# Performance work log

Measured on AMD Instinct MI355X. Metric: run time of the kernel, lower is better.

## Reference

```python
import jax, jax.numpy as jnp
import numpy as np

H, DH, M, ITERS, DIM = 8, 64, 256, 6, 512
SCALE = DH ** -0.5


def setup_inputs() -> dict:
    key = jax.random.key(0)
    ks = jax.random.split(key, 6)
    b, n, nz = 4, 8192, 4096  # multiples of M=256 -> padding branch is a no-op
    s = DIM ** -0.5
    x = jax.random.normal(ks[0], (b, n, DIM), jnp.float32)
    z = jax.random.normal(ks[1], (b, nz, DIM), jnp.float32)
    W_q = jax.random.normal(ks[2], (DIM, H * DH), jnp.float32) * s      # to_qkv[0] (no bias)
    W_kv = jax.random.normal(ks[3], (DIM, 2 * H * DH), jnp.float32) * s  # to_qkv[1] (no bias)
    W_out = jax.random.normal(ks[4], (H * DH, DIM), jnp.float32) * s     # to_out Linear
    b_out = jax.random.normal(ks[5], (DIM,), jnp.float32) * 0.01
    return {"x": x, "z": z, "W_q": W_q, "W_kv": W_kv, "W_out": W_out, "b_out": b_out}


def moore_penrose_pinv(a, iters=ITERS):
    # Newton-Schulz iterative pseudo-inverse (faithful to moore_penrose_iter_pinv)
    abs_a = jnp.abs(a)
    col = abs_a.sum(axis=-1)
    row = abs_a.sum(axis=-2)
    zt = jnp.swapaxes(a, -1, -2) / (jnp.max(col) * jnp.max(row))
    I = jnp.eye(a.shape[-1], dtype=a.dtype)
    for _ in range(iters):
        az = a @ zt
        zt = 0.25 * zt @ (13.0 * I - az @ (15.0 * I - az @ (7.0 * I - az)))
    return zt


def reference(x, z, W_q, W_kv, W_out, b_out):
    b, n, _ = x.shape
    nz = z.shape[1]
    l, lz = n // M, nz // M  # landmark group sizes (n, nz are multiples of M)

    # projections (dropout=0.1 is inactive at inference; self.norm is never applied in forward)
    q = (x @ W_q).reshape(b, n, H, DH).transpose(0, 2, 1, 3) * SCALE   # [b,h,n,dh]
    kv = z @ W_kv
    k = kv[..., : H * DH].reshape(b, nz, H, DH).transpose(0, 2, 1, 3)  # [b,h,nz,dh]
    v = kv[..., H * DH :].reshape(b, nz, H, DH).transpose(0, 2, 1, 3)  # [b,h,nz,dh]

    # landmarks: mean over groups of l (resp. lz) consecutive tokens
    q_land = q.reshape(b, H, M, l, DH).sum(axis=3) / l    # [b,h,M,dh]
    k_land = k.reshape(b, H, M, lz, DH).sum(axis=3) / lz  # [b,h,M,dh]

    sim1 = jnp.einsum('bhid,bhjd->bhij', q, k_land)       # [b,h,n,M]
    sim2 = jnp.einsum('bhid,bhjd->bhij', q_land, k_land)  # [b,h,M,M]
    sim3 = jnp.einsum('bhid,bhjd->bhij', q_land, k)       # [b,h,M,nz]
    attn1 = jax.nn.softmax(sim1, axis=-1)
    attn2 = jax.nn.softmax(sim2, axis=-1)
    attn3 = jax.nn.softmax(sim3, axis=-1)

    attn2_inv = moore_penrose_pinv(attn2)
    # (attn1 @ attn2_inv) @ (attn3 @ v) computed small-first for efficiency; same math
    out = attn1 @ (attn2_inv @ (attn3 @ v))               # [b,h,n,dh]  (residual=False)

    out = out.transpose(0, 2, 1, 3).reshape(b, n, H * DH)
    out = out @ W_out + b_out
    return x + out
```

## Files before the change

### kernel.cpp

```cpp
#include <hip/hip_runtime.h>

typedef unsigned short u16;
typedef __attribute__((ext_vector_type(8))) short bf16x8s;
typedef __attribute__((ext_vector_type(4))) float f32x4;

#define DEV static __device__ __forceinline__

DEV float b2f(u16 v) { return __uint_as_float(((unsigned)v) << 16); }
DEV u16 f2b(float f) {
  unsigned r;
  asm("v_cvt_pk_bf16_f32 %0, %1, %1" : "=v"(r) : "v"(f));
  return (u16)r;
}
DEV unsigned f2b2(float a, float b) {
  unsigned r;
  asm("v_cvt_pk_bf16_f32 %0, %1, %2" : "=v"(r) : "v"(a), "v"(b));
  return r;
}

#define GLL(gp, lp)                                                            \
  __builtin_amdgcn_global_load_lds(                                            \
      (const __attribute__((address_space(1))) unsigned int*)(gp),             \
      (__attribute__((address_space(3))) unsigned int*)(lp), 16, 0, 0)

#define MFMA __builtin_amdgcn_mfma_f32_16x16x32_bf16

__global__ __launch_bounds__(256) void k_f2bxz(const float* __restrict__ x,
                                               const float* __restrict__ z,
                                               u16* __restrict__ xb,
                                               u16* __restrict__ zb) {
  long i = (long)blockIdx.x * 256 + threadIdx.x;
  const float* src;
  u16* dst;
  long j;
  if (i < 4194304) { src = x; dst = xb; j = i; }
  else { src = z; dst = zb; j = i - 4194304; }
  float4 v = *(const float4*)(src + j * 4);
  unsigned* d = (unsigned*)(dst + j * 4);
  d[0] = f2b2(v.x, v.y);
  d[1] = f2b2(v.z, v.w);
}

__global__ __launch_bounds__(256) void k_wt3(const float* __restrict__ Wq,
                                             const float* __restrict__ Wkv,
                                             const float* __restrict__ Wo,
                                             u16* __restrict__ wqt,
                                             u16* __restrict__ wkvt,
                                             u16* __restrict__ wot) {
  int e = blockIdx.x * 256 + threadIdx.x;
  const float* W;
  u16* Wt;
  int N, le;
  if (e < 262144) { W = Wq; Wt = wqt; N = 512; le = e; }
  else if (e < 786432) { W = Wkv; Wt = wkvt; N = 1024; le = e - 262144; }
  else { W = Wo; Wt = wot; N = 512; le = e - 786432; }
  int nn = le >> 9, kk = le & 511;
  Wt[le] = f2b(W[(long)kk * N + nn]);
}

template <int MODE>
__global__ __launch_bounds__(256, 2) void k_gemm128(
    const u16* __restrict__ A, const u16* __restrict__ Bm, void* __restrict__ C0,
    void* __restrict__ C1, const float* __restrict__ xres,
    const float* __restrict__ bias, int K) {
  const int nwg = gridDim.x * gridDim.y;
  const int orig = blockIdx.y * gridDim.x + blockIdx.x;
  const int qq = nwg >> 3, rr = nwg & 7;
  const int xcd = orig & 7, loc = orig >> 3;
  const int swz = (xcd < rr ? xcd * (qq + 1) : rr * (qq + 1) + (xcd - rr) * qq) + loc;
  const int m0 = (swz / gridDim.x) << 7, n0 = (swz % gridDim.x) << 7;
  const int t = threadIdx.x, lane = t & 63, w = t >> 6;
  const int wm = (w >> 1) << 6, wn = (w & 1) << 6;
  const int fr = lane & 15, g = lane >> 4;
  __shared__ u16 sh[16384];
  u16* As = sh;
  u16* Bs = sh + 8192;
  f32x4 acc[4][4] = {};
  const int srow = t >> 3, scs = t & 7;
  for (int k0 = 0; k0 < K; k0 += 64) {
    __syncthreads();
#pragma unroll
    for (int i = 0; i < 4; ++i) {
      int row = srow + (i << 5), cs = scs;
      GLL(A + (long)(m0 + row) * K + k0 + ((cs ^ (row & 7)) << 3),
          &As[(i << 11) + (w << 9)]);
      GLL(Bm + (long)(n0 + row) * K + k0 + ((cs ^ (row & 7)) << 3),
          &Bs[(i << 11) + (w << 9)]);
    }
    __syncthreads();
#pragma unroll
    for (int ks = 0; ks < 2; ++ks) {
      bf16x8s af[4], bf[4];
#pragma unroll
      for (int fi = 0; fi < 4; ++fi) {
        int row = wm + fi * 16 + fr;
        af[fi] = *(const bf16x8s*)((const char*)As + row * 128 +
                                   (((ks * 4 + g) ^ (row & 7)) << 4));
      }
#pragma unroll
      for (int fj = 0; fj < 4; ++fj) {
        int row = wn + fj * 16 + fr;
        bf[fj] = *(const bf16x8s*)((const char*)Bs + row * 128 +
                                   (((ks * 4 + g) ^ (row & 7)) << 4));
      }
#pragma unroll
      for (int fi = 0; fi < 4; ++fi)
#pragma unroll
        for (int fj = 0; fj < 4; ++fj)
          acc[fi][fj] = MFMA(af[fi], bf[fj], acc[fi][fj], 0, 0, 0);
    }
  }
  const int crow = g << 2;
  if (MODE == 2) {
#pragma unroll
    for (int fi = 0; fi < 4; ++fi)
#pragma unroll
      for (int fj = 0; fj < 4; ++fj)
#pragma unroll
        for (int r = 0; r < 4; ++r) {
          int row = m0 + wm + fi * 16 + crow + r;
          int col = n0 + wn + fj * 16 + fr;
          long idx = ((long)row << 9) + col;
          ((float*)C0)[idx] = acc[fi][fj][r] + xres[idx] + bias[col];
        }
  } else {
    __syncthreads();
    char* Cs = (char*)sh;
    const float scale = (MODE == 0) ? 0.125f : 1.f;
#pragma unroll
    for (int fi = 0; fi < 4; ++fi)
#pragma unroll
      for (int fj = 0; fj < 4; ++fj)
#pragma unroll
        for (int r = 0; r < 4; ++r) {
          int row = wm + fi * 16 + crow + r;
          int colb = (wn + fj * 16 + fr) << 1;
          *(u16*)(Cs + ((row * 256 + colb) ^ ((row & 7) << 4))) =
              f2b(acc[fi][fj][r] * scale);
        }
    __syncthreads();
    const bool vt = (MODE == 1) && (n0 >= 512);
    if (!vt) {
#pragma unroll
      for (int i = 0; i < 8; ++i) {
        int seg = (i << 8) + t;
        int row = seg >> 4, cs = seg & 15;
        bf16x8s v = *(const bf16x8s*)(Cs +
                        ((row * 256 + (cs << 4)) ^ ((row & 7) << 4)));
        int m = m0 + row;
        int colg = n0 + (cs << 3);
        int h = colg >> 6, dh0 = colg & 63;
        if (MODE == 0) {
          int b = m >> 13, n = m & 8191;
          *(bf16x8s*)((u16*)C0 + ((((long)(b * 8 + h)) << 13) + n) * 64 + dh0) = v;
        } else {
          int b = m >> 12, nz = m & 4095;
          *(bf16x8s*)((u16*)C0 + ((((long)(b * 8 + h)) << 12) + nz) * 64 + dh0) = v;
        }
      }
    } else {
#pragma unroll
      for (int i = 0; i < 8; ++i) {
        int seg = (i << 8) + t;
        int col = seg & 127;
        int r0 = (seg >> 7) << 3;
        bf16x8s v;
#pragma unroll
        for (int j = 0; j < 8; ++j) {
          int rr = r0 + j;
          v[j] = *(const short*)(Cs + ((rr * 256 + (col << 1)) ^ ((rr & 7) << 4)));
        }
        int m = m0 + r0;
        int b = m >> 12, nz0 = m & 4095;
        int c2 = n0 + col - 512;
        int h = c2 >> 6, dh = c2 & 63;
        *(bf16x8s*)((u16*)C1 + ((((long)(b * 8 + h) * 64 + dh)) << 12) + nz0) = v;
      }
    }
  }
}

__global__ __launch_bounds__(256) void k_land2(const u16* __restrict__ qb,
                                               const u16* __restrict__ kb,
                                               u16* __restrict__ qlh,
                                               u16* __restrict__ qll,
                                               u16* __restrict__ klh,
                                               u16* __restrict__ kll) {
  int pidx = blockIdx.x * 4 + (threadIdx.x >> 6);
  const u16* src;
  u16 *hi, *lo;
  int ntok, l;
  float inv;
  if (pidx < 8192) { src = qb; hi = qlh; lo = qll; ntok = 8192; l = 32; inv = 1.f / 32.f; }
  else { src = kb; hi = klh; lo = kll; ntok = 4096; l = 16; inv = 1.f / 16.f; pidx -= 8192; }
  int d = threadIdx.x & 63;
  int bh = pidx >> 8, m = pidx & 255;
  const u16* s = src + ((long)bh * ntok + (long)m * l) * 64 + d;
  float sum = 0.f;
  for (int j = 0; j < l; ++j) sum += b2f(s[j * 64]);
  sum *= inv;
  long o = ((long)bh * 256 + m) * 64 + d;
  u16 h = f2b(sum);
  hi[o] = h;
  lo[o] = f2b(sum - b2f(h));
}

__global__ __launch_bounds__(256, 2) void k_sim2(
    const u16* __restrict__ qlh, const u16* __restrict__ qll,
    const u16* __restrict__ klh, const u16* __restrict__ kll,
    float* __restrict__ attn2, u16* __restrict__ aNhi, u16* __restrict__ aNlo) {
  const int rb = blockIdx.x, bh = blockIdx.y;
  const int t = threadIdx.x, lane = t & 63, w = t >> 6;
  const int fr = lane & 15, g = lane >> 4;
  __shared__ char lds[65536];
  {
    const u16* kh = klh + (long)bh * 16384;
    const u16* kl = kll + (long)bh * 16384;
    int srow8 = lane >> 3, cs7 = lane & 7;
#pragma unroll
    for (int i = 0; i < 8; ++i) {
      int slab = w * 8 + i;
      int krow = slab * 8 + srow8;
      GLL(kh + krow * 64 + ((cs7 ^ (krow & 7)) << 3), lds + slab * 1024);
      GLL(kl + krow * 64 + ((cs7 ^ (krow & 7)) << 3), lds + 32768 + slab * 1024);
    }
  }
  long qoff = ((long)bh * 256 + rb * 64 + w * 16 + fr) * 64;
  bf16x8s qh0 = *(const bf16x8s*)(qlh + qoff + g * 8);
  bf16x8s qh1 = *(const bf16x8s*)(qlh + qoff + 32 + g * 8);
  bf16x8s ql0 = *(const bf16x8s*)(qll + qoff + g * 8);
  bf16x8s ql1 = *(const bf16x8s*)(qll + qoff + 32 + g * 8);
  __syncthreads();
  f32x4 s[16];
#pragma unroll
  for (int c = 0; c < 16; ++c) {
    int j = (c << 4) + fr;
    int o0 = j * 128 + ((g ^ (j & 7)) << 4);
    int o1 = j * 128 + (((4 + g) ^ (j & 7)) << 4);
    bf16x8s kh0 = *(const bf16x8s*)(lds + o0);
    bf16x8s kh1 = *(const bf16x8s*)(lds + o1);
    bf16x8s kl0 = *(const bf16x8s*)(lds + 32768 + o0);
    bf16x8s kl1 = *(const bf16x8s*)(lds + 32768 + o1);
    f32x4 zz = {};
    zz = MFMA(qh0, kh0, zz, 0, 0, 0);
    zz = MFMA(qh1, kh1, zz, 0, 0, 0);
    zz = MFMA(qh0, kl0, zz, 0, 0, 0);
    zz = MFMA(qh1, kl1, zz, 0, 0, 0);
    zz = MFMA(ql0, kh0, zz, 0, 0, 0);
    zz = MFMA(ql1, kh1, zz, 0, 0, 0);
    s[c] = zz;
  }
  float li[4];
#pragma unroll
  for (int r = 0; r < 4; ++r) {
    float m = s[0][r];
#pragma unroll
    for (int c = 1; c < 16; ++c) m = fmaxf(m, s[c][r]);
    m = fmaxf(m, __shfl_xor(m, 1, 64));
    m = fmaxf(m, __shfl_xor(m, 2, 64));
    m = fmaxf(m, __shfl_xor(m, 4, 64));
    m = fmaxf(m, __shfl_xor(m, 8, 64));
    float l = 0.f;
#pragma unroll
    for (int c = 0; c < 16; ++c) {
      float e = __expf(s[c][r] - m);
      s[c][r] = e;
      l += e;
    }
    l += __shfl_xor(l, 1, 64);
    l += __shfl_xor(l, 2, 64);
    l += __shfl_xor(l, 4, 64);
    l += __shfl_xor(l, 8, 64);
    li[r] = 1.f / l;
  }
#pragma unroll
  for (int c = 0; c < 16; ++c)
#pragma unroll
    for (int r = 0; r < 4; ++r) {
      int row = rb * 64 + w * 16 + (g << 2) + r;
      int col = (c << 4) + fr;
      long idx = ((long)bh << 16) + ((long)row << 8) + col;
      float p = s[c][r] * li[r];
      attn2[idx] = p;
      u16 h = f2b(p);
      aNhi[idx] = h;
      aNlo[idx] = f2b(p - b2f(h));
    }
}

__global__ __launch_bounds__(256) void k_colmax(const float* __restrict__ attn2,
                                                unsigned* __restrict__ cmax) {
  int bh = blockIdx.x, j = threadIdx.x, lane = j & 63, w = j >> 6;
  const float* p = attn2 + ((long)bh << 16) + j;
  float s = 0.f;
  for (int m = 0; m < 256; ++m) s += p[m * 256];
  float mx = s;
  for (int o = 1; o < 64; o <<= 1) mx = fmaxf(mx, __shfl_xor(mx, o, 64));
  __shared__ float r1[4];
  if (lane == 0) r1[w] = mx;
  __syncthreads();
  if (j == 0) {
    mx = fmaxf(fmaxf(r1[0], r1[1]), fmaxf(r1[2], r1[3]));
    atomicMax(cmax, __float_as_uint(mx));
  }
}

__global__ __launch_bounds__(256, 2) void k_t1part(
    const u16* __restrict__ qlb, const u16* __restrict__ kb,
    const u16* __restrict__ vtb, float* __restrict__ opart,
    float* __restrict__ pm_, float* __restrict__ pl_) {
  int orig = blockIdx.x;
  int xcd = orig & 7, idx = orig >> 3;
  int p = xcd * 16 + (idx >> 2);
  int rb = idx & 3;
  int bh = p >> 2, kc = p & 3;
  const int t = threadIdx.x, lane = t & 63, w = t >> 6;
  const int fr = lane & 15, g = lane >> 4;
  __shared__ char lds[65536];
  const u16* qrow = qlb + ((long)bh * 256 + rb * 64 + w * 16 + fr) * 64;
  bf16x8s qa0 = *(const bf16x8s*)(qrow + g * 8);
  bf16x8s qa1 = *(const bf16x8s*)(qrow + 32 + g * 8);
  f32x4 o[4] = {};
  float m[4] = {-3e38f, -3e38f, -3e38f, -3e38f};
  float l[4] = {};
  const long kbase = (long)bh * 262144;
  for (int cc = 0; cc < 4; ++cc) {
    int c0 = kc * 1024 + cc * 256;
    __syncthreads();
#pragma unroll
    for (int i = 0; i < 8; ++i) {
      int seg = (i << 8) + t, row = seg >> 3, cs = seg & 7;
      GLL(kb + kbase + (long)(c0 + row) * 64 + ((cs ^ (row & 7)) << 3),
          lds + (i << 12) + (w << 10));
    }
#pragma unroll
    for (int i = 0; i < 8; ++i) {
      int seg = (i << 8) + t, row = seg >> 5, cs = seg & 31;
      GLL(vtb + kbase + (long)row * 4096 + c0 + ((cs ^ (row & 7)) << 3),
          lds + 32768 + (i << 12) + (w << 10));
    }
    __syncthreads();
    f32x4 s[16];
#pragma unroll
    for (int c = 0; c < 16; ++c) {
      int j = c * 16 + fr;
      bf16x8s b0 = *(const bf16x8s*)(lds + j * 128 + ((g ^ (j & 7)) << 4));
      bf16x8s b1 = *(const bf16x8s*)(lds + j * 128 + (((4 + g) ^ (j & 7)) << 4));
      f32x4 zz = {};
      zz = MFMA(qa0, b0, zz, 0, 0, 0);
      zz = MFMA(qa1, b1, zz, 0, 0, 0);
      s[c] = zz;
    }
    float sc[4];
#pragma unroll
    for (int r = 0; r < 4; ++r) {
      float pm = s[0][r];
#pragma unroll
      for (int c = 1; c < 16; ++c) pm = fmaxf(pm, s[c][r]);
      pm = fmaxf(pm, __shfl_xor(pm, 1, 64));
      pm = fmaxf(pm, __shfl_xor(pm, 2, 64));
      pm = fmaxf(pm, __shfl_xor(pm, 4, 64));
      pm = fmaxf(pm, __shfl_xor(pm, 8, 64));
      float mn = fmaxf(m[r], pm);
      sc[r] = __expf(m[r] - mn);
      m[r] = mn;
    }
#pragma unroll
    for (int r = 0; r < 4; ++r) {
      float su = 0.f;
#pragma unroll
      for (int c = 0; c < 16; ++c) {
        float e = __expf(s[c][r] - m[r]);
        s[c][r] = e;
        su += e;
      }
      su += __shfl_xor(su, 1, 64);
      su += __shfl_xor(su, 2, 64);
      su += __shfl_xor(su, 4, 64);
      su += __shfl_xor(su, 8, 64);
      l[r] = l[r] * sc[r] + su;
    }
#pragma unroll
    for (int d = 0; d < 4; ++d)
#pragma unroll
      for (int r = 0; r < 4; ++r) o[d][r] *= sc[r];
    __syncthreads();
#pragma unroll
    for (int c = 0; c < 16; ++c)
#pragma unroll
      for (int r = 0; r < 4; ++r) {
        int row = (w << 4) + (g << 2) + r;
        int byin = (c << 5) + (fr << 1);
        *(u16*)(lds + row * 512 + (byin ^ ((row & 7) << 4))) = f2b(s[c][r]);
      }
    asm volatile("s_waitcnt lgkmcnt(0)" ::: "memory");
    __builtin_amdgcn_sched_barrier(0);
#pragma unroll
    for (int ss = 0; ss < 8; ++ss) {
      int prow = (w << 4) + fr;
      bf16x8s ap = *(const bf16x8s*)(lds + prow * 512 +
                                     (((ss * 64) + (g << 4)) ^ ((prow & 7) << 4)));
#pragma unroll
      for (int d = 0; d < 4; ++d) {
        int dh = (d << 4) + fr;
        bf16x8s bv = *(const bf16x8s*)(lds + 32768 + dh * 512 +
                                       (((ss * 4 + g) ^ (dh & 7)) << 4));
        o[d] = MFMA(ap, bv, o[d], 0, 0, 0);
      }
    }
  }
  __syncthreads();
  float* lf = (float*)lds;
#pragma unroll
  for (int d = 0; d < 4; ++d)
#pragma unroll
    for (int r = 0; r < 4; ++r)
      lf[((w << 4) + (g << 2) + r) * 76 + (d << 4) + fr] = o[d][r];
  __syncthreads();
  const long pb = (long)(bh * 4 + kc) * 256 + rb * 64;
#pragma unroll
  for (int i = 0; i < 4; ++i) {
    int row = i * 16 + (t >> 4);
    int c4 = (t & 15) << 2;
    float4 v = *(const float4*)&lf[row * 76 + c4];
    *(float4*)&opart[(pb + row) * 64 + c4] = v;
  }
  if (fr == 0) {
#pragma unroll
    for (int r = 0; r < 4; ++r) {
      int lr = (w << 4) + (g << 2) + r;
      pm_[pb + lr] = m[r];
      pl_[pb + lr] = l[r];
    }
  }
}

__global__ __launch_bounds__(256) void k_t1merge(
    const float* __restrict__ opart, const float* __restrict__ pm_,
    const float* __restrict__ pl_, u16* __restrict__ T1thi,
    u16* __restrict__ T1tlo) {
  const int rb = blockIdx.x, bh = blockIdx.y;
  const int t = threadIdx.x;
#pragma unroll
  for (int rp = 0; rp < 4; ++rp) {
    int row = rb * 64 + rp * 16 + (t >> 4);
    int dh4 = (t & 15) << 2;
    float pmv[4], M = -3e38f;
#pragma unroll
    for (int i = 0; i < 4; ++i) {
      pmv[i] = pm_[(long)(bh * 4 + i) * 256 + row];
      M = fmaxf(M, pmv[i]);
    }
    float L = 0.f, wt[4];
#pragma unroll
    for (int i = 0; i < 4; ++i) {
      wt[i] = __expf(pmv[i] - M);
      L += pl_[(long)(bh * 4 + i) * 256 + row] * wt[i];
    }
    float4 acc = {0.f, 0.f, 0.f, 0.f};
#pragma unroll
    for (int i = 0; i < 4; ++i) {
      float4 v = *(const float4*)&opart[((long)(bh * 4 + i) * 256 + row) * 64 + dh4];
      acc.x += v.x * wt[i]; acc.y += v.y * wt[i];
      acc.z += v.z * wt[i]; acc.w += v.w * wt[i];
    }
    float invL = 1.f / L;
    float vv[4] = {acc.x * invL, acc.y * invL, acc.z * invL, acc.w * invL};
#pragma unroll
    for (int e = 0; e < 4; ++e) {
      int dh = dh4 + e;
      long idx = (long)bh * 16384 + (long)dh * 256 + row;
      u16 h = f2b(vv[e]);
      T1thi[idx] = h;
      T1tlo[idx] = f2b(vv[e] - b2f(h));
    }
  }
}

template <int NP>
__global__ __launch_bounds__(256) void k_nn_mfma(
    const u16* __restrict__ Ahi, const u16* __restrict__ Alo,
    const u16* __restrict__ Bthi, const u16* __restrict__ Btlo,
    u16* __restrict__ CNhi, u16* __restrict__ CNlo,
    u16* __restrict__ CThi, u16* __restrict__ CTlo,
    int Nc, float sab, float sa, float cdiag) {
  const int bz = blockIdx.z;
  const long offA = (long)bz << 16;
  const long offB = (long)bz * ((long)Nc << 8);
  const int m0 = blockIdx.y << 6, n0 = blockIdx.x << 6;
  const int t = threadIdx.x, lane = t & 63, w = t >> 6;
  const int wm = (w >> 1) << 5, wn = (w & 1) << 5;
  const int fr = lane & 15, g = lane >> 4;
  __shared__ u16 lds[16384];
  u16* LAh = lds;
  u16* LAl = lds + 4096;
  u16* LBh = lds + 8192;
  u16* LBl = lds + 12288;
  f32x4 acc[2][2] = {};
  const int srow8 = lane >> 3, cs = lane & 7;
  for (int k0 = 0; k0 < 256; k0 += 64) {
    __syncthreads();
#pragma unroll
    for (int j = 0; j < 2; ++j) {
      int slab = w * 2 + j;
      int row = slab * 8 + srow8;
      long asrc = offA + (long)(m0 + row) * 256 + k0 + ((cs ^ (row & 7)) << 3);
      long bsrc = offB + (long)(n0 + row) * 256 + k0 + ((cs ^ (row & 7)) << 3);
      GLL(Ahi + asrc, LAh + slab * 512);
      GLL(Bthi + bsrc, LBh + slab * 512);
      if (NP == 3) {
        GLL(Alo + asrc, LAl + slab * 512);
        GLL(Btlo + bsrc, LBl + slab * 512);
      }
    }
    __syncthreads();
#pragma unroll
    for (int ks = 0; ks < 2; ++ks) {
      const int ra0 = wm + fr, ra1 = wm + 16 + fr;
      const int rb0 = wn + fr, rb1 = wn + 16 + fr;
#define RD(base, row) \
  (*(const bf16x8s*)((const char*)(base) + (row) * 128 + (((ks * 4 + g) ^ ((row) & 7)) << 4)))
      bf16x8s ah0 = RD(LAh, ra0), ah1 = RD(LAh, ra1);
      bf16x8s bh0 = RD(LBh, rb0), bh1 = RD(LBh, rb1);
      acc[0][0] = MFMA(ah0, bh0, acc[0][0], 0, 0, 0);
      acc[0][1] = MFMA(ah0, bh1, acc[0][1], 0, 0, 0);
      acc[1][0] = MFMA(ah1, bh0, acc[1][0], 0, 0, 0);
      acc[1][1] = MFMA(ah1, bh1, acc[1][1], 0, 0, 0);
      if (NP == 3) {
        bf16x8s al0 = RD(LAl, ra0), al1 = RD(LAl, ra1);
        bf16x8s bl0 = RD(LBl, rb0), bl1 = RD(LBl, rb1);
        acc[0][0] = MFMA(ah0, bl0, acc[0][0], 0, 0, 0);
        acc[0][0] = MFMA(al0, bh0, acc[0][0], 0, 0, 0);
        acc[0][1] = MFMA(ah0, bl1, acc[0][1], 0, 0, 0);
        acc[0][1] = MFMA(al0, bh1, acc[0][1], 0, 0, 0);
        acc[1][0] = MFMA(ah1, bl0, acc[1][0], 0, 0, 0);
        acc[1][0] = MFMA(al1, bh0, acc[1][0], 0, 0, 0);
        acc[1][1] = MFMA(ah1, bl1, acc[1][1], 0, 0, 0);
        acc[1][1] = MFMA(al1, bh1, acc[1][1], 0, 0, 0);
      }
#undef RD
    }
  }
  const int crow = g << 2;
  const long offC = (long)bz * ((long)Nc << 8);
#pragma unroll
  for (int i = 0; i < 2; ++i)
#pragma unroll
    for (int j = 0; j < 2; ++j)
#pragma unroll
      for (int r = 0; r < 4; ++r) {
        int row = m0 + wm + i * 16 + crow + r;
        int col = n0 + wn + j * 16 + fr;
        float v = sab * acc[i][j][r];
        if (sa != 0.f) {
          long ai = offA + ((long)row << 8) + col;
          v += sa * (b2f(Ahi[ai]) + b2f(Alo[ai]));
        }
        if (row == col) v += cdiag;
        if (CNhi) {
          long ci = offC + (long)row * Nc + col;
          u16 h = f2b(v);
          if (CNlo) { CNhi[ci] = h; CNlo[ci] = f2b(v - b2f(h)); }
          else CNhi[ci] = h;
        }
        if (CThi) {
          long ti = offC + ((long)col << 8) + row;
          u16 h = f2b(v);
          CThi[ti] = h;
          if (CTlo) CTlo[ti] = f2b(v - b2f(h));
        }
      }
}

__global__ __launch_bounds__(256) void k_prep_pinv(
    const float* __restrict__ attn2, const unsigned* __restrict__ cmax,
    u16* __restrict__ zNhi, u16* __restrict__ zNlo,
    u16* __restrict__ zThi, u16* __restrict__ zTlo) {
  const int bz = blockIdx.z, i0 = blockIdx.y << 6, j0 = blockIdx.x << 6;
  const float s = 1.f / __uint_as_float(*cmax);
  const float* base = attn2 + ((long)bz << 16);
  __shared__ float mt[64][65];
  const int r = threadIdx.x >> 2, cb = (threadIdx.x & 3) << 4;
#pragma unroll
  for (int c4 = 0; c4 < 16; c4 += 4) {
    float4 v = *(const float4*)&base[(long)(j0 + r) * 256 + i0 + cb + c4];
    mt[r][cb + c4] = v.x; mt[r][cb + c4 + 1] = v.y;
    mt[r][cb + c4 + 2] = v.z; mt[r][cb + c4 + 3] = v.w;
  }
  __syncthreads();
  const int i = i0 + r;
#pragma unroll
  for (int c4 = 0; c4 < 16; c4 += 4) {
    float4 v = *(const float4*)&base[(long)i * 256 + j0 + cb + c4];
    float vv[4] = {v.x, v.y, v.z, v.w};
#pragma unroll
    for (int e = 0; e < 4; ++e) {
      int j = j0 + cb + c4 + e;
      long idx = ((long)bz << 16) + ((long)i << 8) + j;
      float zt = vv[e] * s;
      u16 zh = f2b(zt);
      zThi[idx] = zh; zTlo[idx] = f2b(zt - b2f(zh));
      float zn = mt[cb + c4 + e][r] * s;
      u16 nh = f2b(zn);
      zNhi[idx] = nh; zNlo[idx] = f2b(zn - b2f(nh));
    }
  }
}

__global__ __launch_bounds__(512, 4) void k_fused_attn1(const u16* __restrict__ q,
                                                        const u16* __restrict__ klb,
                                                        const u16* __restrict__ t2t,
                                                        u16* __restrict__ O) {
  const int bh = blockIdx.y, n0 = blockIdx.x << 7;
  const int bb = bh >> 3, hh = bh & 7;
  const int t = threadIdx.x, lane = t & 63, w = t >> 6;
  const int fr = lane & 15, g = lane >> 4;
  __shared__ char lds[65536];
  {
    const u16* ks = klb + (long)bh * 16384;
    const u16* ts = t2t + (long)bh * 16384;
#pragma unroll
    for (int i = 0; i < 4; ++i) {
      int seg = (i << 9) + t, row = seg >> 3, cs = seg & 7;
      GLL(ks + row * 64 + ((cs ^ (row & 7)) << 3), lds + (i << 13) + (w << 10));
      int slab = w * 4 + i;
      int trow = slab * 2 + (lane >> 5), cs32 = lane & 31;
      GLL(ts + trow * 256 + ((cs32 ^ (trow & 7)) << 3),
          lds + 32768 + slab * 1024);
    }
  }
  __syncthreads();
  const u16* qrow = q + ((long)bh * 8192 + n0 + (w << 4) + fr) * 64;
  bf16x8s qa0 = *(const bf16x8s*)(qrow + g * 8);
  bf16x8s qa1 = *(const bf16x8s*)(qrow + 32 + g * 8);
  f32x4 s[16];
#pragma unroll
  for (int c = 0; c < 16; ++c) {
    int j = (c << 4) + fr;
    bf16x8s b0 = *(const bf16x8s*)(lds + j * 128 + ((g ^ (j & 7)) << 4));
    bf16x8s b1 = *(const bf16x8s*)(lds + j * 128 + (((4 + g) ^ (j & 7)) << 4));
    f32x4 zz = {};
    zz = MFMA(qa0, b0, zz, 0, 0, 0);
    zz = MFMA(qa1, b1, zz, 0, 0, 0);
    s[c] = zz;
  }
  float li[4];
#pragma unroll
  for (int r = 0; r < 4; ++r) {
    float m = s[0][r];
#pragma unroll
    for (int c = 1; c < 16; ++c) m = fmaxf(m, s[c][r]);
    m = fmaxf(m, __shfl_xor(m, 1, 64));
    m = fmaxf(m, __shfl_xor(m, 2, 64));
    m = fmaxf(m, __shfl_xor(m, 4, 64));
    m = fmaxf(m, __shfl_xor(m, 8, 64));
    float l = 0.f;
#pragma unroll
    for (int c = 0; c < 16; ++c) {
      float e = __expf(s[c][r] - m);
      s[c][r] = e;
      l += e;
    }
    l += __shfl_xor(l, 1, 64);
    l += __shfl_xor(l, 2, 64);
    l += __shfl_xor(l, 4, 64);
    l += __shfl_xor(l, 8, 64);
    li[r] = 1.f / l;
  }
  __syncthreads();
  f32x4 o4[4] = {};
#pragma unroll
  for (int p = 0; p < 2; ++p) {
#pragma unroll
    for (int c8 = 0; c8 < 8; ++c8) {
      int c = p * 8 + c8;
#pragma unroll
      for (int r = 0; r < 4; ++r) {
        int row = (w << 4) + (g << 2) + r;
        int byin = (c8 << 5) + (fr << 1);
        *(u16*)(lds + row * 256 + (byin ^ ((row & 7) << 4))) = f2b(s[c][r]);
      }
    }
    asm volatile("s_waitcnt lgkmcnt(0)" ::: "memory");
    __builtin_amdgcn_sched_barrier(0);
#pragma unroll
    for (int ss8 = 0; ss8 < 4; ++ss8) {
      int ss = p * 4 + ss8;
      int prow = (w << 4) + fr;
      bf16x8s ap = *(const bf16x8s*)(lds + prow * 256 +
                                     (((ss8 * 64) + (g << 4)) ^ ((prow & 7) << 4)));
#pragma unroll
      for (int d = 0; d < 4; ++d) {
        int dh = (d << 4) + fr;
        bf16x8s bv = *(const bf16x8s*)(lds + 32768 + dh * 512 +
                                       (((ss * 4 + g) ^ (dh & 7)) << 4));
        o4[d] = MFMA(ap, bv, o4[d], 0, 0, 0);
      }
    }
    asm volatile("s_waitcnt lgkmcnt(0)" ::: "memory");
    __builtin_amdgcn_sched_barrier(0);
  }
  u16* ob = O + (((long)bb * 8192 + n0 + (w << 4)) << 9) + (hh << 6);
#pragma unroll
  for (int d = 0; d < 4; ++d)
#pragma unroll
    for (int r = 0; r < 4; ++r) {
      int row = (g << 2) + r;
      int col = (d << 4) + fr;
      ob[((long)row << 9) + col] = f2b(o4[d][r] * li[r]);
    }
}

extern "C" void kernel_launch(void* const* d_in, const int* in_sizes, int n_in,
                              void* d_out, int out_size, void* d_ws, size_t ws_size,
                              hipStream_t stream) {
  const float* x = (const float*)d_in[0];
  const float* z = (const float*)d_in[1];
  const float* Wq = (const float*)d_in[2];
  const float* Wkv = (const float*)d_in[3];
  const float* Wo = (const float*)d_in[4];
  const float* bo = (const float*)d_in[5];
  float* out = (float*)d_out;

  char* base = (char*)d_ws;
  size_t off = 0;
  auto alloc = [&](size_t bytes) -> void* {
    void* r = base + off;
    off = (off + bytes + 255) & ~(size_t)255;
    return r;
  };
  u16* qb = (u16*)alloc(33554432);
  u16* kb = (u16*)alloc(16777216);
  u16* vtb = (u16*)alloc(16777216);
  u16* PS = (u16*)alloc(67108864);
  float* attn2 = (float*)alloc(8388608);
  u16* xb = (u16*)alloc(33554432);
  u16* zb = (u16*)alloc(16777216);
  u16* wqt = (u16*)alloc(524288);
  u16* wkvt = (u16*)alloc(1048576);
  u16* wot = (u16*)alloc(524288);
  u16* qlh = (u16*)alloc(1048576);
  u16* qll = (u16*)alloc(1048576);
  u16* klh = (u16*)alloc(1048576);
  u16* kll = (u16*)alloc(1048576);
  u16* T1t = (u16*)alloc(2097152);
  u16* T2t = (u16*)alloc(1048576);
  unsigned* cmax = (unsigned*)alloc(256);
  const long MC = 2097152;
  u16* P = PS;
  u16 *ztA_Nhi = P,          *ztA_Nlo = P + MC,      *ztA_Thi = P + 2 * MC,  *ztA_Tlo = P + 3 * MC;
  u16 *ztB_Nhi = P + 4 * MC,  *ztB_Nlo = P + 5 * MC,  *ztB_Thi = P + 6 * MC,  *ztB_Tlo = P + 7 * MC;
  u16 *az_Nhi = P + 8 * MC,   *az_Nlo = P + 9 * MC,   *az_Thi = P + 10 * MC,  *az_Tlo = P + 11 * MC;
  u16 *taThi = P + 12 * MC,   *taTlo = P + 13 * MC;
  u16 *tcThi = P + 14 * MC,   *tcTlo = P + 15 * MC;
  u16 *aNhi = zb, *aNlo = zb + MC;
  float* opart = (float*)PS;
  float* pm_ = opart + 2097152;
  float* pl_ = pm_ + 32768;
  u16* T1thi = T1t;
  u16* T1tlo = T1t + 524288;
  u16* Ob = xb;

  hipMemsetAsync(cmax, 0, 4, stream);
  k_f2bxz<<<24576, 256, 0, stream>>>(x, z, xb, zb);
  k_wt3<<<4096, 256, 0, stream>>>(Wq, Wkv, Wo, wqt, wkvt, wot);

  k_gemm128<0><<<dim3(4, 256), 256, 0, stream>>>(xb, wqt, qb, nullptr, nullptr,
                                                 nullptr, 512);
  k_gemm128<1><<<dim3(8, 128), 256, 0, stream>>>(zb, wkvt, kb, vtb, nullptr,
                                                 nullptr, 512);
  k_land2<<<4096, 256, 0, stream>>>(qb, kb, qlh, qll, klh, kll);

  k_sim2<<<dim3(4, 32), 256, 0, stream>>>(qlh, qll, klh, kll, attn2, aNhi, aNlo);
  k_colmax<<<32, 256, 0, stream>>>(attn2, cmax);

  k_t1part<<<512, 256, 0, stream>>>(qlh, kb, vtb, opart, pm_, pl_);
  k_t1merge<<<dim3(4, 32), 256, 0, stream>>>(opart, pm_, pl_, T1thi, T1tlo);

  k_prep_pinv<<<dim3(4, 4, 32), 256, 0, stream>>>(attn2, cmax, ztA_Nhi, ztA_Nlo,
                                                  ztA_Thi, ztA_Tlo);

  dim3 g256(4, 4, 32);
  u16 *cN0 = ztA_Nhi, *cN1 = ztA_Nlo, *cT0 = ztA_Thi, *cT1 = ztA_Tlo;
  u16 *nN0 = ztB_Nhi, *nN1 = ztB_Nlo, *nT0 = ztB_Thi, *nT1 = ztB_Tlo;
  for (int it = 0; it < 6; ++it) {
    bool last = (it == 5);
    if (it < 5) {
      k_nn_mfma<1><<<g256, 256, 0, stream>>>(aNhi, aNlo, cT0, cT1, az_Nhi, az_Nlo,
                                             az_Thi, az_Tlo, 256, 1.f, 0.f, 0.f);
      k_nn_mfma<1><<<g256, 256, 0, stream>>>(az_Nhi, az_Nlo, az_Thi, az_Tlo, nullptr,
                                             nullptr, taThi, taTlo, 256, 1.f, -7.f, 15.f);
      k_nn_mfma<1><<<g256, 256, 0, stream>>>(az_Nhi, az_Nlo, taThi, taTlo, nullptr,
                                             nullptr, tcThi, tcTlo, 256, -1.f, 0.f, 13.f);
      k_nn_mfma<1><<<g256, 256, 0, stream>>>(cN0, cN1, tcThi, tcTlo, nN0, nN1,
                                             nT0, nT1, 256, 0.25f, 0.f, 0.f);
    } else {
      k_nn_mfma<3><<<g256, 256, 0, stream>>>(aNhi, aNlo, cT0, cT1, az_Nhi, az_Nlo,
                                             az_Thi, az_Tlo, 256, 1.f, 0.f, 0.f);
      k_nn_mfma<3><<<g256, 256, 0, stream>>>(az_Nhi, az_Nlo, az_Thi, az_Tlo, nullptr,
                                             nullptr, taThi, taTlo, 256, 1.f, -7.f, 15.f);
      k_nn_mfma<3><<<g256, 256, 0, stream>>>(az_Nhi, az_Nlo, taThi, taTlo, nullptr,
                                             nullptr, tcThi, tcTlo, 256, -1.f, 0.f, 13.f);
      k_nn_mfma<3><<<g256, 256, 0, stream>>>(cN0, cN1, tcThi, tcTlo, nN0, nN1,
                                             last ? nullptr : nT0, last ? nullptr : nT1,
                                             256, 0.25f, 0.f, 0.f);
    }
    u16* t0;
    t0 = cN0; cN0 = nN0; nN0 = t0;  t0 = cN1; cN1 = nN1; nN1 = t0;
    t0 = cT0; cT0 = nT0; nT0 = t0;  t0 = cT1; cT1 = nT1; nT1 = t0;
  }
  k_nn_mfma<3><<<dim3(1, 4, 32), 256, 0, stream>>>(cN0, cN1, T1thi, T1tlo, nullptr,
                                                   nullptr, T2t, nullptr, 64,
                                                   1.f, 0.f, 0.f);

  k_fused_attn1<<<dim3(64, 32), 512, 0, stream>>>(qb, klh, T2t, Ob);
  k_gemm128<2><<<dim3(4, 256), 256, 0, stream>>>(Ob, wot, out, nullptr, x, bo, 512);
}
```

Before: 595.0 us.

## Merge small prep kernels into combined launches and deepen pinv GEMM K-tile

Several independent small kernels are merged into shared launches that branch on block index: the input and weight bf16 conversion, the column-max with the T1 partial attention, and the T1 merge with the pinv init. The opart scratch moves into the xb buffer so it no longer aliases the pinv buffers, which lets the merge and the pinv init run in one launch. The Newton-Schulz GEMM now loads K in 128-wide chunks with a new swizzle, halving its barrier rounds, and the NP=3 variant doubles its LDS. This cuts launch and serialization overhead but may lower occupancy and adds branch divergence across blocks.

```diff
diff --git a/kernel.cpp b/kernel.cpp
--- a/kernel.cpp
+++ b/kernel.cpp
@@ -25,37 +25,38 @@
 
 #define MFMA __builtin_amdgcn_mfma_f32_16x16x32_bf16
 
-__global__ __launch_bounds__(256) void k_f2bxz(const float* __restrict__ x,
-                                               const float* __restrict__ z,
-                                               u16* __restrict__ xb,
-                                               u16* __restrict__ zb) {
-  long i = (long)blockIdx.x * 256 + threadIdx.x;
-  const float* src;
-  u16* dst;
-  long j;
-  if (i < 4194304) { src = x; dst = xb; j = i; }
-  else { src = z; dst = zb; j = i - 4194304; }
-  float4 v = *(const float4*)(src + j * 4);
-  unsigned* d = (unsigned*)(dst + j * 4);
-  d[0] = f2b2(v.x, v.y);
-  d[1] = f2b2(v.z, v.w);
-}
-
-__global__ __launch_bounds__(256) void k_wt3(const float* __restrict__ Wq,
+__global__ __launch_bounds__(256) void k_pre(const float* __restrict__ x,
+                                             const float* __restrict__ z,
+                                             u16* __restrict__ xb,
+                                             u16* __restrict__ zb,
+                                             const float* __restrict__ Wq,
                                              const float* __restrict__ Wkv,
                                              const float* __restrict__ Wo,
                                              u16* __restrict__ wqt,
                                              u16* __restrict__ wkvt,
                                              u16* __restrict__ wot) {
-  int e = blockIdx.x * 256 + threadIdx.x;
-  const float* W;
-  u16* Wt;
-  int N, le;
-  if (e < 262144) { W = Wq; Wt = wqt; N = 512; le = e; }
-  else if (e < 786432) { W = Wkv; Wt = wkvt; N = 1024; le = e - 262144; }
-  else { W = Wo; Wt = wot; N = 512; le = e - 786432; }
-  int nn = le >> 9, kk = le & 511;
-  Wt[le] = f2b(W[(long)kk * N + nn]);
+  if (blockIdx.x < 24576) {
+    long i = (long)blockIdx.x * 256 + threadIdx.x;
+    const float* src;
+    u16* dst;
+    long j;
+    if (i < 4194304) { src = x; dst = xb; j = i; }
+    else { src = z; dst = zb; j = i - 4194304; }
+    float4 v = *(const float4*)(src + j * 4);
+    unsigned* d = (unsigned*)(dst + j * 4);
+    d[0] = f2b2(v.x, v.y);
+    d[1] = f2b2(v.z, v.w);
+  } else {
+    int e = (blockIdx.x - 24576) * 256 + threadIdx.x;
+    const float* W;
+    u16* Wt;
+    int N, le;
+    if (e < 262144) { W = Wq; Wt = wqt; N = 512; le = e; }
+    else if (e < 786432) { W = Wkv; Wt = wkvt; N = 1024; le = e - 262144; }
+    else { W = Wo; Wt = wot; N = 512; le = e - 786432; }
+    int nn = le >> 9, kk = le & 511;
+    Wt[le] = f2b(W[(long)kk * N + nn]);
+  }
 }
 
 template <int MODE>
@@ -288,35 +289,35 @@
     }
 }
 
-__global__ __launch_bounds__(256) void k_colmax(const float* __restrict__ attn2,
-                                                unsigned* __restrict__ cmax) {
-  int bh = blockIdx.x, j = threadIdx.x, lane = j & 63, w = j >> 6;
-  const float* p = attn2 + ((long)bh << 16) + j;
-  float s = 0.f;
-  for (int m = 0; m < 256; ++m) s += p[m * 256];
-  float mx = s;
-  for (int o = 1; o < 64; o <<= 1) mx = fmaxf(mx, __shfl_xor(mx, o, 64));
-  __shared__ float r1[4];
-  if (lane == 0) r1[w] = mx;
-  __syncthreads();
-  if (j == 0) {
-    mx = fmaxf(fmaxf(r1[0], r1[1]), fmaxf(r1[2], r1[3]));
-    atomicMax(cmax, __float_as_uint(mx));
-  }
-}
-
-__global__ __launch_bounds__(256, 2) void k_t1part(
+__global__ __launch_bounds__(256, 2) void k_cm_t1(
+    const float* __restrict__ attn2, unsigned* __restrict__ cmax,
     const u16* __restrict__ qlb, const u16* __restrict__ kb,
     const u16* __restrict__ vtb, float* __restrict__ opart,
     float* __restrict__ pm_, float* __restrict__ pl_) {
-  int orig = blockIdx.x;
+  __shared__ char lds[65536];
+  if (blockIdx.x < 32) {
+    int bh = blockIdx.x, j = threadIdx.x, lane = j & 63, w = j >> 6;
+    const float* p = attn2 + ((long)bh << 16) + j;
+    float s = 0.f;
+    for (int m = 0; m < 256; ++m) s += p[m * 256];
+    float mx = s;
+    for (int o = 1; o < 64; o <<= 1) mx = fmaxf(mx, __shfl_xor(mx, o, 64));
+    float* r1 = (float*)lds;
+    if (lane == 0) r1[w] = mx;
+    __syncthreads();
+    if (j == 0) {
+      mx = fmaxf(fmaxf(r1[0], r1[1]), fmaxf(r1[2], r1[3]));
+      atomicMax(cmax, __float_as_uint(mx));
+    }
+    return;
+  }
+  int orig = blockIdx.x - 32;
   int xcd = orig & 7, idx = orig >> 3;
   int p = xcd * 16 + (idx >> 2);
   int rb = idx & 3;
   int bh = p >> 2, kc = p & 3;
   const int t = threadIdx.x, lane = t & 63, w = t >> 6;
   const int fr = lane & 15, g = lane >> 4;
-  __shared__ char lds[65536];
   const u16* qrow = qlb + ((long)bh * 256 + rb * 64 + w * 16 + fr) * 64;
   bf16x8s qa0 = *(const bf16x8s*)(qrow + g * 8);
   bf16x8s qa1 = *(const bf16x8s*)(qrow + 32 + g * 8);
@@ -435,44 +436,79 @@
   }
 }
 
-__global__ __launch_bounds__(256) void k_t1merge(
+__global__ __launch_bounds__(256) void k_mergeprep(
     const float* __restrict__ opart, const float* __restrict__ pm_,
     const float* __restrict__ pl_, u16* __restrict__ T1thi,
-    u16* __restrict__ T1tlo) {
-  const int rb = blockIdx.x, bh = blockIdx.y;
-  const int t = threadIdx.x;
-#pragma unroll
-  for (int rp = 0; rp < 4; ++rp) {
-    int row = rb * 64 + rp * 16 + (t >> 4);
-    int dh4 = (t & 15) << 2;
-    float pmv[4], M = -3e38f;
-#pragma unroll
-    for (int i = 0; i < 4; ++i) {
-      pmv[i] = pm_[(long)(bh * 4 + i) * 256 + row];
-      M = fmaxf(M, pmv[i]);
-    }
-    float L = 0.f, wt[4];
-#pragma unroll
-    for (int i = 0; i < 4; ++i) {
-      wt[i] = __expf(pmv[i] - M);
-      L += pl_[(long)(bh * 4 + i) * 256 + row] * wt[i];
-    }
-    float4 acc = {0.f, 0.f, 0.f, 0.f};
-#pragma unroll
-    for (int i = 0; i < 4; ++i) {
-      float4 v = *(const float4*)&opart[((long)(bh * 4 + i) * 256 + row) * 64 + dh4];
-      acc.x += v.x * wt[i]; acc.y += v.y * wt[i];
-      acc.z += v.z * wt[i]; acc.w += v.w * wt[i];
-    }
-    float invL = 1.f / L;
-    float vv[4] = {acc.x * invL, acc.y * invL, acc.z * invL, acc.w * invL};
+    u16* __restrict__ T1tlo, const float* __restrict__ attn2,
+    const unsigned* __restrict__ cmax, u16* __restrict__ zNhi,
+    u16* __restrict__ zNlo, u16* __restrict__ zThi, u16* __restrict__ zTlo) {
+  __shared__ float mt[64][65];
+  if (blockIdx.x < 128) {
+    const int rb = blockIdx.x & 3, bh = blockIdx.x >> 2;
+    const int t = threadIdx.x;
+#pragma unroll
+    for (int rp = 0; rp < 4; ++rp) {
+      int row = rb * 64 + rp * 16 + (t >> 4);
+      int dh4 = (t & 15) << 2;
+      float pmv[4], M = -3e38f;
+#pragma unroll
+      for (int i = 0; i < 4; ++i) {
+        pmv[i] = pm_[(long)(bh * 4 + i) * 256 + row];
+        M = fmaxf(M, pmv[i]);
+      }
+      float L = 0.f, wt[4];
+#pragma unroll
+      for (int i = 0; i < 4; ++i) {
+        wt[i] = __expf(pmv[i] - M);
+        L += pl_[(long)(bh * 4 + i) * 256 + row] * wt[i];
+      }
+      float4 acc = {0.f, 0.f, 0.f, 0.f};
+#pragma unroll
+      for (int i = 0; i < 4; ++i) {
+        float4 v = *(const float4*)&opart[((long)(bh * 4 + i) * 256 + row) * 64 + dh4];
+        acc.x += v.x * wt[i]; acc.y += v.y * wt[i];
+        acc.z += v.z * wt[i]; acc.w += v.w * wt[i];
+      }
+      float invL = 1.f / L;
+      float vv[4] = {acc.x * invL, acc.y * invL, acc.z * invL, acc.w * invL};
+#pragma unroll
+      for (int e = 0; e < 4; ++e) {
+        int dh = dh4 + e;
+        long idx = (long)bh * 16384 + (long)dh * 256 + row;
+        u16 h = f2b(vv[e]);
+        T1thi[idx] = h;
+        T1tlo[idx] = f2b(vv[e] - b2f(h));
+      }
+    }
+    return;
+  }
+  const int p = blockIdx.x - 128;
+  const int bz = p >> 4, i0 = ((p >> 2) & 3) << 6, j0 = (p & 3) << 6;
+  const float s = 1.f / __uint_as_float(*cmax);
+  const float* base = attn2 + ((long)bz << 16);
+  const int r = threadIdx.x >> 2, cb = (threadIdx.x & 3) << 4;
+#pragma unroll
+  for (int c4 = 0; c4 < 16; c4 += 4) {
+    float4 v = *(const float4*)&base[(long)(j0 + r) * 256 + i0 + cb + c4];
+    mt[r][cb + c4] = v.x; mt[r][cb + c4 + 1] = v.y;
+    mt[r][cb + c4 + 2] = v.z; mt[r][cb + c4 + 3] = v.w;
+  }
+  __syncthreads();
+  const int i = i0 + r;
+#pragma unroll
+  for (int c4 = 0; c4 < 16; c4 += 4) {
+    float4 v = *(const float4*)&base[(long)i * 256 + j0 + cb + c4];
+    float vv[4] = {v.x, v.y, v.z, v.w};
 #pragma unroll
     for (int e = 0; e < 4; ++e) {
-      int dh = dh4 + e;
-      long idx = (long)bh * 16384 + (long)dh * 256 + row;
-      u16 h = f2b(vv[e]);
-      T1thi[idx] = h;
-      T1tlo[idx] = f2b(vv[e] - b2f(h));
+      int j = j0 + cb + c4 + e;
+      long idx = ((long)bz << 16) + ((long)i << 8) + j;
+      float zt = vv[e] * s;
+      u16 zh = f2b(zt);
+      zThi[idx] = zh; zTlo[idx] = f2b(zt - b2f(zh));
+      float zn = mt[cb + c4 + e][r] * s;
+      u16 nh = f2b(zn);
+      zNhi[idx] = nh; zNlo[idx] = f2b(zn - b2f(nh));
     }
   }
 }
@@ -491,35 +527,37 @@
   const int t = threadIdx.x, lane = t & 63, w = t >> 6;
   const int wm = (w >> 1) << 5, wn = (w & 1) << 5;
   const int fr = lane & 15, g = lane >> 4;
-  __shared__ u16 lds[16384];
+  __shared__ u16 lds[(NP == 3) ? 32768 : 16384];
   u16* LAh = lds;
-  u16* LAl = lds + 4096;
   u16* LBh = lds + 8192;
-  u16* LBl = lds + 12288;
+  u16* LAl = (NP == 3) ? lds + 16384 : nullptr;
+  u16* LBl = (NP == 3) ? lds + 24576 : nullptr;
   f32x4 acc[2][2] = {};
-  const int srow8 = lane >> 3, cs = lane & 7;
-  for (int k0 = 0; k0 < 256; k0 += 64) {
-    __syncthreads();
-#pragma unroll
-    for (int j = 0; j < 2; ++j) {
-      int slab = w * 2 + j;
-      int row = slab * 8 + srow8;
-      long asrc = offA + (long)(m0 + row) * 256 + k0 + ((cs ^ (row & 7)) << 3);
-      long bsrc = offB + (long)(n0 + row) * 256 + k0 + ((cs ^ (row & 7)) << 3);
-      GLL(Ahi + asrc, LAh + slab * 512);
-      GLL(Bthi + bsrc, LBh + slab * 512);
+  for (int k0 = 0; k0 < 256; k0 += 128) {
+    __syncthreads();
+#pragma unroll
+    for (int i = 0; i < 4; ++i) {
+      int row = (i << 4) + (t >> 4);
+      int sp = t & 15;
+      int seg = (sp & 8) | ((sp & 7) ^ (row & 7));
+      long asrc = offA + (long)(m0 + row) * 256 + k0 + (seg << 3);
+      long bsrc = offB + (long)(n0 + row) * 256 + k0 + (seg << 3);
+      GLL(Ahi + asrc, (char*)LAh + (i << 12) + (w << 10));
+      GLL(Bthi + bsrc, (char*)LBh + (i << 12) + (w << 10));
       if (NP == 3) {
-        GLL(Alo + asrc, LAl + slab * 512);
-        GLL(Btlo + bsrc, LBl + slab * 512);
-      }
-    }
-    __syncthreads();
-#pragma unroll
-    for (int ks = 0; ks < 2; ++ks) {
+        GLL(Alo + asrc, (char*)LAl + (i << 12) + (w << 10));
+        GLL(Btlo + bsrc, (char*)LBl + (i << 12) + (w << 10));
+      }
+    }
+    __syncthreads();
+#pragma unroll
+    for (int ks = 0; ks < 4; ++ks) {
       const int ra0 = wm + fr, ra1 = wm + 16 + fr;
       const int rb0 = wn + fr, rb1 = wn + 16 + fr;
-#define RD(base, row) \
-  (*(const bf16x8s*)((const char*)(base) + (row) * 128 + (((ks * 4 + g) ^ ((row) & 7)) << 4)))
+#define RD(base, row)                                                          \
+  (*(const bf16x8s*)((const char*)(base) + (row) * 256 +                       \
+                     ((((ks * 4 + g) & 8) |                                    \
+                       (((ks * 4 + g) & 7) ^ ((row) & 7))) << 4)))
       bf16x8s ah0 = RD(LAh, ra0), ah1 = RD(LAh, ra1);
       bf16x8s bh0 = RD(LBh, rb0), bh1 = RD(LBh, rb1);
       acc[0][0] = MFMA(ah0, bh0, acc[0][0], 0, 0, 0);
@@ -570,41 +608,6 @@
           if (CTlo) CTlo[ti] = f2b(v - b2f(h));
         }
       }
-}
-
-__global__ __launch_bounds__(256) void k_prep_pinv(
-    const float* __restrict__ attn2, const unsigned* __restrict__ cmax,
-    u16* __restrict__ zNhi, u16* __restrict__ zNlo,
-    u16* __restrict__ zThi, u16* __restrict__ zTlo) {
-  const int bz = blockIdx.z, i0 = blockIdx.y << 6, j0 = blockIdx.x << 6;
-  const float s = 1.f / __uint_as_float(*cmax);
-  const float* base = attn2 + ((long)bz << 16);
-  __shared__ float mt[64][65];
-  const int r = threadIdx.x >> 2, cb = (threadIdx.x & 3) << 4;
-#pragma unroll
-  for (int c4 = 0; c4 < 16; c4 += 4) {
-    float4 v = *(const float4*)&base[(long)(j0 + r) * 256 + i0 + cb + c4];
-    mt[r][cb + c4] = v.x; mt[r][cb + c4 + 1] = v.y;
-    mt[r][cb + c4 + 2] = v.z; mt[r][cb + c4 + 3] = v.w;
-  }
-  __syncthreads();
-  const int i = i0 + r;
-#pragma unroll
-  for (int c4 = 0; c4 < 16; c4 += 4) {
-    float4 v = *(const float4*)&base[(long)i * 256 + j0 + cb + c4];
-    float vv[4] = {v.x, v.y, v.z, v.w};
-#pragma unroll
-    for (int e = 0; e < 4; ++e) {
-      int j = j0 + cb + c4 + e;
-      long idx = ((long)bz << 16) + ((long)i << 8) + j;
-      float zt = vv[e] * s;
-      u16 zh = f2b(zt);
-      zThi[idx] = zh; zTlo[idx] = f2b(zt - b2f(zh));
-      float zn = mt[cb + c4 + e][r] * s;
-      u16 nh = f2b(zn);
-      zNhi[idx] = nh; zNlo[idx] = f2b(zn - b2f(nh));
-    }
-  }
 }
 
 __global__ __launch_bounds__(512, 4) void k_fused_attn1(const u16* __restrict__ q,
@@ -754,7 +757,7 @@
   u16 *taThi = P + 12 * MC,   *taTlo = P + 13 * MC;
   u16 *tcThi = P + 14 * MC,   *tcTlo = P + 15 * MC;
   u16 *aNhi = zb, *aNlo = zb + MC;
-  float* opart = (float*)PS;
+  float* opart = (float*)xb;
   float* pm_ = opart + 2097152;
   float* pl_ = pm_ + 32768;
   u16* T1thi = T1t;
@@ -762,8 +765,7 @@
   u16* Ob = xb;
 
   hipMemsetAsync(cmax, 0, 4, stream);
-  k_f2bxz<<<24576, 256, 0, stream>>>(x, z, xb, zb);
-  k_wt3<<<4096, 256, 0, stream>>>(Wq, Wkv, Wo, wqt, wkvt, wot);
+  k_pre<<<28672, 256, 0, stream>>>(x, z, xb, zb, Wq, Wkv, Wo, wqt, wkvt, wot);
 
   k_gemm128<0><<<dim3(4, 256), 256, 0, stream>>>(xb, wqt, qb, nullptr, nullptr,
                                                  nullptr, 512);
@@ -772,13 +774,10 @@
   k_land2<<<4096, 256, 0, stream>>>(qb, kb, qlh, qll, klh, kll);
 
   k_sim2<<<dim3(4, 32), 256, 0, stream>>>(qlh, qll, klh, kll, attn2, aNhi, aNlo);
-  k_colmax<<<32, 256, 0, stream>>>(attn2, cmax);
-
-  k_t1part<<<512, 256, 0, stream>>>(qlh, kb, vtb, opart, pm_, pl_);
-  k_t1merge<<<dim3(4, 32), 256, 0, stream>>>(opart, pm_, pl_, T1thi, T1tlo);
-
-  k_prep_pinv<<<dim3(4, 4, 32), 256, 0, stream>>>(attn2, cmax, ztA_Nhi, ztA_Nlo,
-                                                  ztA_Thi, ztA_Tlo);
+
+  k_cm_t1<<<544, 256, 0, stream>>>(attn2, cmax, qlh, kb, vtb, opart, pm_, pl_);
+  k_mergeprep<<<640, 256, 0, stream>>>(opart, pm_, pl_, T1thi, T1tlo, attn2,
+                                       cmax, ztA_Nhi, ztA_Nlo, ztA_Thi, ztA_Tlo);
 
   dim3 g256(4, 4, 32);
   u16 *cN0 = ztA_Nhi, *cN1 = ztA_Nlo, *cT0 = ztA_Thi, *cT1 = ztA_Tlo;
```

New measurement: 593.3 us. No clear change (-0.3%).
